# Performance work log

Hardware: AMD Instinct MI355X
Metric: run time of the kernel (lower is better)

## Reference

```python
import jax, jax.numpy as jnp
import numpy as np

B, S, HID = 1, 2048, 4096
NH, NKV, HD = 32, 8, 128
GROUPS = NH // NKV
EPS = 1e-8
THETA = 10000.0
SCALE = HD ** -0.5
INIT = 0.02


def setup_inputs() -> dict:
    key = jax.random.key(0)
    ks = jax.random.split(key, 8)
    return {
        "hidden_states": jax.random.normal(ks[0], (B, S, HID), jnp.float32),
        "position_ids": jnp.arange(S, dtype=jnp.int32)[None, :],
        "wq": jax.random.normal(ks[1], (HID, NH * HD), jnp.float32) * INIT,
        "wk": jax.random.normal(ks[2], (HID, NKV * HD), jnp.float32) * INIT,
        "wv": jax.random.normal(ks[3], (HID, NKV * HD), jnp.float32) * INIT,
        "wo": jax.random.normal(ks[4], (NH * HD, HID), jnp.float32) * INIT,
        "memory": jax.random.normal(ks[5], (NKV, HD, HD), jnp.float32) * INIT,
        "norm_m": jax.random.uniform(ks[6], (NKV, HD, HD), jnp.float32) * 0.5 + 0.5,
        "beta": jnp.zeros((1,), jnp.float32),
    }


def _rotate_half(x):
    h = x.shape[-1] // 2
    return jnp.concatenate([-x[..., h:], x[..., :h]], axis=-1)


def _rope(position_ids):
    inv_freq = 1.0 / (THETA ** (jnp.arange(0, HD, 2, dtype=jnp.float32) / HD))  # [HD/2]
    freqs = position_ids.astype(jnp.float32)[:, :, None] * inv_freq[None, None, :]  # [B,S,HD/2]
    emb = jnp.concatenate([freqs, freqs], axis=-1)  # [B,S,HD]
    return jnp.cos(emb)[:, None], jnp.sin(emb)[:, None]  # [B,1,S,HD] each


def reference(hidden_states, position_ids, wq, wk, wv, wo, memory, norm_m, beta):
    # projections -> [B, heads, S, HD]
    q = (hidden_states @ wq).reshape(B, S, NH, HD).transpose(0, 2, 1, 3)
    k = (hidden_states @ wk).reshape(B, S, NKV, HD).transpose(0, 2, 1, 3)
    v = (hidden_states @ wv).reshape(B, S, NKV, HD).transpose(0, 2, 1, 3)

    # ---- retrieve from compressive memory (pre-RoPE Q, as in original) ----
    qf = jax.nn.elu(q) + 1.0
    qn = qf / (qf.sum(axis=-1, keepdims=True) + EPS)            # [B,NH,S,HD]
    mem_t = jnp.tile(memory[None], (1, GROUPS, 1, 1))            # torch .repeat == tile: head h -> memory[h % NKV]
    norm_t = jnp.tile(jnp.swapaxes(norm_m, -1, -2)[None], (1, GROUPS, 1, 1))
    mem_out = jnp.matmul(qn, mem_t) / (jnp.matmul(qn, norm_t) + EPS)  # [B,NH,S,HD]

    # ---- delta-rule memory update (no-grad side effect in torch) ----
    kf = jax.nn.elu(k) + 1.0
    kn = kf / (kf.sum(axis=-1, keepdims=True) + EPS)             # [B,NKV,S,HD]
    v_ret = jnp.matmul(kn, memory) / (jnp.matmul(kn, jnp.swapaxes(norm_m, -1, -2)) + EPS)
    delta = jnp.einsum('bhsd,bhse->hde', kn, v - v_ret)          # sum over batch
    updated_memory = memory + delta
    updated_norm = norm_m + kn.sum(axis=2, keepdims=True)[0]     # [NKV,1,HD] broadcast

    # ---- RoPE ----
    cos, sin = _rope(position_ids)
    q = q * cos + _rotate_half(q) * sin
    k = k * cos + _rotate_half(k) * sin

    # ---- causal attention with GQA (repeat_interleave for K/V) ----
    kr = jnp.repeat(k, GROUPS, axis=1)
    vr = jnp.repeat(v, GROUPS, axis=1)
    scores = jnp.einsum('bhqd,bhkd->bhqk', q, kr) * SCALE        # [B,NH,S,S]
    causal = jnp.tril(jnp.ones((S, S), dtype=bool))
    scores = jnp.where(causal, scores, jnp.finfo(scores.dtype).min)
    attn = jax.nn.softmax(scores, axis=-1)
    attn_out = jnp.einsum('bhqk,bhkd->bhqd', attn, vr)           # [B,NH,S,HD]

    # ---- sigmoid-gated combine + output projection ----
    gate = jax.nn.sigmoid(beta)                                   # [1]
    combined = gate * mem_out + (1.0 - gate) * attn_out
    out = combined.transpose(0, 2, 1, 3).reshape(B, S, NH * HD) @ wo
    return out, updated_memory, updated_norm
```

## Files before the change

kernel.cpp:

```cpp
#include <hip/hip_runtime.h>

#define S_LEN 2048
#define HID_DIM 4096
#define NH 32
#define NKV 8
#define HD 128
#define QKV_N 6144
#define SCALE_F 0.08838834764831845f

typedef unsigned short u16;
typedef __attribute__((ext_vector_type(8))) __bf16 bf16x8;
typedef __attribute__((ext_vector_type(4))) float f32x4;

__device__ __forceinline__ u16 f2bf(float f) {
  unsigned u = __float_as_uint(f);
  return (u16)((u + 0x7fffu + ((u >> 16) & 1u)) >> 16);
}
__device__ __forceinline__ float bf2f(u16 v) {
  return __uint_as_float((unsigned)v << 16);
}

__device__ __forceinline__ void gl_lds16(const u16* g, u16* l) {
  __builtin_amdgcn_global_load_lds(
      (const __attribute__((address_space(1))) unsigned int*)g,
      (__attribute__((address_space(3))) unsigned int*)l, 16, 0, 0);
}


__device__ __forceinline__ void tr64_body(const float* __restrict__ A, u16* __restrict__ O,
                                          int ld_in, int ld_out, int r0, int c0, int tid) {
  __shared__ float tile[64][65];
  int tx = tid & 31, ty = tid >> 5;
#pragma unroll
  for (int i = 0; i < 8; i++) {
    int r = ty + 8 * i;
    float2 v = *(const float2*)&A[(long)(r0 + r) * ld_in + c0 + 2 * tx];
    tile[r][2 * tx] = v.x;
    tile[r][2 * tx + 1] = v.y;
  }
  __syncthreads();
#pragma unroll
  for (int i = 0; i < 8; i++) {
    int c = ty + 8 * i;
    ushort2 o;
    o.x = f2bf(tile[2 * tx][c]);
    o.y = f2bf(tile[2 * tx + 1][c]);
    *(ushort2*)&O[(long)(c0 + c) * ld_out + r0 + 2 * tx] = o;
  }
}

__device__ __forceinline__ void tr64u_body(const u16* __restrict__ A, u16* __restrict__ O,
                                           int ld_in, int ld_out, int r0, int c0, int tid) {
  __shared__ u16 tileu[64][66];
  int tx = tid & 31, ty = tid >> 5;
#pragma unroll
  for (int i = 0; i < 8; i++) {
    int r = ty + 8 * i;
    ushort2 v = *(const ushort2*)&A[(long)(r0 + r) * ld_in + c0 + 2 * tx];
    tileu[r][2 * tx] = v.x;
    tileu[r][2 * tx + 1] = v.y;
  }
  __syncthreads();
#pragma unroll
  for (int i = 0; i < 8; i++) {
    int c = ty + 8 * i;
    ushort2 o;
    o.x = tileu[2 * tx][c];
    o.y = tileu[2 * tx + 1][c];
    *(ushort2*)&O[(long)(c0 + c) * ld_out + r0 + 2 * tx] = o;
  }
}

__global__ void k_tr64(const float* __restrict__ in, u16* __restrict__ out,
                       int ld_in, int ld_out, long in_bs, long out_bs) {
  tr64_body(in + (long)blockIdx.z * in_bs, out + (long)blockIdx.z * out_bs,
            ld_in, ld_out, blockIdx.y * 64, blockIdx.x * 64, threadIdx.x);
}

__global__ void k_prep(const float* __restrict__ hs, u16* __restrict__ hsb,
                       const float* __restrict__ wq, const float* __restrict__ wk,
                       const float* __restrict__ wv, u16* __restrict__ wT6) {
  int bid = blockIdx.x;
  if (bid < 6144) {
    const float* src; int ld, bx, by; long ooff;
    if (bid < 4096) { src = wq; ld = 4096; ooff = 0; bx = bid & 63; by = bid >> 6; }
    else if (bid < 5120) { int b = bid - 4096; src = wk; ld = 1024; ooff = (long)4096 * HID_DIM; bx = b & 15; by = b >> 4; }
    else { int b = bid - 5120; src = wv; ld = 1024; ooff = (long)5120 * HID_DIM; bx = b & 15; by = b >> 4; }
    tr64_body(src, wT6 + ooff, ld, HID_DIM, by * 64, bx * 64, threadIdx.x);
  } else {
    long i = (long)(bid - 6144) * 256 + threadIdx.x;
    float4 v = ((const float4*)hs)[i];
    ushort4 o;
    o.x = f2bf(v.x); o.y = f2bf(v.y); o.z = f2bf(v.z); o.w = f2bf(v.w);
    ((ushort4*)hsb)[i] = o;
  }
}

__global__ void k_mid(const u16* __restrict__ qkvb, u16* __restrict__ vtb,
                      const float* __restrict__ memf, const float* __restrict__ norm,
                      u16* __restrict__ bc) {
  int bid = blockIdx.x;
  if (bid < 512) {
    int z = bid >> 6, sub = bid & 63;
    int bx = sub & 1, by = sub >> 1;
    tr64u_body(qkvb + HID_DIM + NKV * HD + z * HD, vtb + (long)z * HD * S_LEN,
               QKV_N, S_LEN, by * 64, bx * 64, threadIdx.x);
  } else if (bid < 544) {
    int b = bid - 512;
    int h = b >> 2, sub = b & 3;
    tr64_body(memf + (long)h * HD * HD, bc + (long)h * 32768,
              HD, HD, (sub >> 1) * 64, (sub & 1) * 64, threadIdx.x);
  } else {
    int cid = bid - 544;
    int h = cid >> 6, chunk = cid & 63;
    int i = chunk * 256 + threadIdx.x;
    bc[(long)h * 32768 + 16384 + i] = f2bf(norm[(long)h * 16384 + i]);
  }
}


template <int BN>
__global__ __launch_bounds__(512, 2) void k_gemm8(
    const u16* __restrict__ A, const u16* __restrict__ A2, int zsplit,
    const u16* __restrict__ Bt, void* __restrict__ Cv,
    int kloop, int lda, int ldb, int ldc,
    long strideA, long strideB, long strideC, int bmodB, int obf) {
  constexpr int NBG = BN / 64;
  constexpr int NNI = BN / 64;
  constexpr int BSTRIDE = 16384 + BN * 64;
  __shared__ __align__(16) u16 lds[2 * BSTRIDE];
  const int bz = blockIdx.z;
  const u16* Ap = (bz < zsplit) ? (A + (long)bz * strideA)
                                : (A2 + (long)(bz - zsplit) * strideA);
  const u16* Bp = Bt + (long)(bz % bmodB) * strideB;
  const long coff = (long)bz * strideC;

  const int gx = gridDim.x, gy = gridDim.y;
  const int nwg = gx * gy;
  int id = blockIdx.y * gx + blockIdx.x;
  if (!(nwg & 7)) { int q = nwg >> 3; id = (id & 7) * q + (id >> 3); }
  const int m0 = (id % gy) * 256;
  const int n0 = (id / gy) * BN;

  const int tid = threadIdx.x, wid = tid >> 6, lane = tid & 63;
  const int l15 = lane & 15, lhi = lane >> 4;
  const int wm = wid >> 2, wn = wid & 3;

  const int srow = (wid << 3) + (lane >> 3);
  const int ssw = ((lane & 7) ^ (lane >> 3)) * 8;
  auto stA = [&](int d, int g, long kt) {
    gl_lds16(Ap + (long)(m0 + g * 64 + srow) * lda + kt + ssw,
             &lds[d * BSTRIDE + (g * 64 + (wid << 3)) * 64]);
  };
  auto stB = [&](int d, int g, long kt) {
    gl_lds16(Bp + (long)(n0 + g * 64 + srow) * ldb + kt + ssw,
             &lds[d * BSTRIDE + 16384 + (g * 64 + (wid << 3)) * 64]);
  };

  const int swb = l15 & 7;
  const int aBase = (wm * 128 + l15) * 64;
  const int bBase = 16384 + (wn * (BN / 4) + l15) * 64;
  const int ko0 = (lhi ^ swb) * 8;
  const int ko1 = ((4 + lhi) ^ swb) * 8;

  const int KT = kloop >> 6;
  const int NIT = KT >> 1;

  f32x4 acc[8][NNI];
#pragma unroll
  for (int i = 0; i < 8; i++)
#pragma unroll
    for (int j = 0; j < NNI; j++) acc[i][j] = (f32x4){0.f, 0.f, 0.f, 0.f};

#pragma unroll
  for (int g = 0; g < 4; g++) stA(0, g, 0);
#pragma unroll
  for (int g = 0; g < NBG; g++) stB(0, g, 0);
#pragma unroll
  for (int g = 0; g < NBG; g++) stB(1, g, 64);
  asm volatile("s_waitcnt vmcnt(%0)" :: "i"(NBG) : "memory");
  __builtin_amdgcn_s_barrier();
  asm volatile("" ::: "memory");

  for (int t = 0; t < NIT; ++t) {
    const long kA = (long)(2 * t + 1) * 64;
    const long kB0 = (long)(2 * t + 2) * 64;
    const long kB1 = (long)(2 * t + 3) * 64;
    const bool st0 = (2 * t + 2) < KT;
    const bool st1 = (2 * t + 3) < KT;
    const bool last = (t + 1 == NIT);

    {
      const u16* lb = &lds[0];
      bf16x8 Bf[NNI][2];
#pragma unroll
      for (int p = 0; p < 4; p++) {
        if (p == 0) {
#pragma unroll
          for (int ni = 0; ni < NNI; ni++) {
            Bf[ni][0] = *(const bf16x8*)&lb[bBase + ni * 1024 + ko0];
            Bf[ni][1] = *(const bf16x8*)&lb[bBase + ni * 1024 + ko1];
          }
        }
        bf16x8 a0k0 = *(const bf16x8*)&lb[aBase + (2 * p) * 1024 + ko0];
        bf16x8 a0k1 = *(const bf16x8*)&lb[aBase + (2 * p) * 1024 + ko1];
        bf16x8 a1k0 = *(const bf16x8*)&lb[aBase + (2 * p + 1) * 1024 + ko0];
        bf16x8 a1k1 = *(const bf16x8*)&lb[aBase + (2 * p + 1) * 1024 + ko1];
        if (p == 0) { stA(1, 0, kA); stA(1, 1, kA); }
        else if (p == 1) { stA(1, 2, kA); stA(1, 3, kA); }
        else if (p == 2) { if (st0) { stB(0, 0, kB0); stB(0, 1, kB0); } }
        else {
          if (st0) { stB(0, 2, kB0); if (NBG > 3) stB(0, 3, kB0); }
        }
        asm volatile("" ::: "memory");
        if (p == 3) {
          if (last) asm volatile("s_waitcnt vmcnt(0)" ::: "memory");
          else      asm volatile("s_waitcnt vmcnt(%0)" :: "i"(NBG) : "memory");
        }
        __builtin_amdgcn_s_barrier();
        asm volatile("" ::: "memory");
        __builtin_amdgcn_s_setprio(1);
#pragma unroll
        for (int ni = 0; ni < NNI; ni++) {
          acc[2 * p][ni] = __builtin_amdgcn_mfma_f32_16x16x32_bf16(a0k0, Bf[ni][0], acc[2 * p][ni], 0, 0, 0);
          acc[2 * p][ni] = __builtin_amdgcn_mfma_f32_16x16x32_bf16(a0k1, Bf[ni][1], acc[2 * p][ni], 0, 0, 0);
          acc[2 * p + 1][ni] = __builtin_amdgcn_mfma_f32_16x16x32_bf16(a1k0, Bf[ni][0], acc[2 * p + 1][ni], 0, 0, 0);
          acc[2 * p + 1][ni] = __builtin_amdgcn_mfma_f32_16x16x32_bf16(a1k1, Bf[ni][1], acc[2 * p + 1][ni], 0, 0, 0);
        }
        __builtin_amdgcn_s_setprio(0);
        asm volatile("" ::: "memory");
        __builtin_amdgcn_s_barrier();
        asm volatile("" ::: "memory");
      }
    }
    {
      const u16* lb = &lds[BSTRIDE];
      bf16x8 Bf[NNI][2];
#pragma unroll
      for (int p = 0; p < 4; p++) {
        if (p == 0) {
#pragma unroll
          for (int ni = 0; ni < NNI; ni++) {
            Bf[ni][0] = *(const bf16x8*)&lb[bBase + ni * 1024 + ko0];
            Bf[ni][1] = *(const bf16x8*)&lb[bBase + ni * 1024 + ko1];
          }
        }
        bf16x8 a0k0 = *(const bf16x8*)&lb[aBase + (2 * p) * 1024 + ko0];
        bf16x8 a0k1 = *(const bf16x8*)&lb[aBase + (2 * p) * 1024 + ko1];
        bf16x8 a1k0 = *(const bf16x8*)&lb[aBase + (2 * p + 1) * 1024 + ko0];
        bf16x8 a1k1 = *(const bf16x8*)&lb[aBase + (2 * p + 1) * 1024 + ko1];
        if (p == 0) { if (st0) { stA(0, 0, kB0); stA(0, 1, kB0); } }
        else if (p == 1) { if (st0) { stA(0, 2, kB0); stA(0, 3, kB0); } }
        else if (p == 2) { if (st1) { stB(1, 0, kB1); stB(1, 1, kB1); } }
        else {
          if (st1) { stB(1, 2, kB1); if (NBG > 3) stB(1, 3, kB1); }
        }
        asm volatile("" ::: "memory");
        if (p == 3 && !last)
          asm volatile("s_waitcnt vmcnt(%0)" :: "i"(NBG) : "memory");
        __builtin_amdgcn_s_barrier();
        asm volatile("" ::: "memory");
        __builtin_amdgcn_s_setprio(1);
#pragma unroll
        for (int ni = 0; ni < NNI; ni++) {
          acc[2 * p][ni] = __builtin_amdgcn_mfma_f32_16x16x32_bf16(a0k0, Bf[ni][0], acc[2 * p][ni], 0, 0, 0);
          acc[2 * p][ni] = __builtin_amdgcn_mfma_f32_16x16x32_bf16(a0k1, Bf[ni][1], acc[2 * p][ni], 0, 0, 0);
          acc[2 * p + 1][ni] = __builtin_amdgcn_mfma_f32_16x16x32_bf16(a1k0, Bf[ni][0], acc[2 * p + 1][ni], 0, 0, 0);
          acc[2 * p + 1][ni] = __builtin_amdgcn_mfma_f32_16x16x32_bf16(a1k1, Bf[ni][1], acc[2 * p + 1][ni], 0, 0, 0);
        }
        __builtin_amdgcn_s_setprio(0);
        asm volatile("" ::: "memory");
        __builtin_amdgcn_s_barrier();
        asm volatile("" ::: "memory");
      }
    }
  }

#pragma unroll
  for (int mi = 0; mi < 8; mi++)
#pragma unroll
    for (int ni = 0; ni < NNI; ni++)
#pragma unroll
      for (int j = 0; j < 4; j++) {
        long row = m0 + wm * 128 + mi * 16 + lhi * 4 + j;
        long col = n0 + wn * (BN / 4) + ni * 16 + l15;
        if (obf)
          ((u16*)Cv)[coff + row * ldc + col] = f2bf(acc[mi][ni][j]);
        else
          ((float*)Cv)[coff + row * ldc + col] = acc[mi][ni][j];
      }
}


__global__ void k_addp(const u16* __restrict__ p0, const u16* __restrict__ p1,
                       float* __restrict__ out) {
  long i = ((long)blockIdx.x * 256 + threadIdx.x) * 8;
  ushort4 a0 = *(const ushort4*)&p0[i], a1 = *(const ushort4*)&p0[i + 4];
  ushort4 b0 = *(const ushort4*)&p1[i], b1 = *(const ushort4*)&p1[i + 4];
  float4 o0, o1;
  o0.x = bf2f(a0.x) + bf2f(b0.x); o0.y = bf2f(a0.y) + bf2f(b0.y);
  o0.z = bf2f(a0.z) + bf2f(b0.z); o0.w = bf2f(a0.w) + bf2f(b0.w);
  o1.x = bf2f(a1.x) + bf2f(b1.x); o1.y = bf2f(a1.y) + bf2f(b1.y);
  o1.z = bf2f(a1.z) + bf2f(b1.z); o1.w = bf2f(a1.w) + bf2f(b1.w);
  *(float4*)&out[i] = o0;
  *(float4*)&out[i + 4] = o1;
}


__global__ void k_qnrope(const u16* __restrict__ qkv, const int* __restrict__ pos,
                         u16* __restrict__ qnb, u16* __restrict__ qrb,
                         u16* __restrict__ knb, u16* __restrict__ krb) {
  int s = blockIdx.x, y = blockIdx.y, l = threadIdx.x;
  bool isq = y < NH;
  int h = isq ? y : y - NH;
  const u16* row = qkv + (long)s * QKV_N + (isq ? h * HD : HID_DIM + h * HD);
  float x0 = bf2f(row[l]), x1 = bf2f(row[l + 64]);
  float f0 = x0 > 0.f ? x0 + 1.f : __expf(x0);
  float f1 = x1 > 0.f ? x1 + 1.f : __expf(x1);
  float sum = f0 + f1;
#pragma unroll
  for (int m = 32; m >= 1; m >>= 1) sum += __shfl_xor(sum, m);
  float inv = 1.f / (sum + 1e-8f);
  float y0 = f0 * inv, y1 = f1 * inv;
  long o = ((long)h * S_LEN + s) * HD;
  float p = (float)pos[s];
  float ang = p * expf(-(float)l * (9.210340371976184f / 64.0f));
  float c = cosf(ang), sn = sinf(ang);
  u16 r0 = f2bf(x0 * c - x1 * sn), r1 = f2bf(x1 * c + x0 * sn);
  if (isq) {
    qnb[o + l] = f2bf(y0); qnb[o + l + 64] = f2bf(y1);
    qrb[o + l] = r0; qrb[o + l + 64] = r1;
  } else {
    knb[o + l] = f2bf(y0); knb[o + l + 64] = f2bf(y1);
    krb[o + l] = r0; krb[o + l + 64] = r1;
  }
}


__global__ __launch_bounds__(256, 2) void k_flash4(
    const u16* __restrict__ qr, const u16* __restrict__ kr,
    const u16* __restrict__ vt, const u16* __restrict__ rawq,
    const float* __restrict__ beta, u16* __restrict__ comb) {
  __shared__ u16 KV[2][16384];
  __shared__ u16 Ps[4][16 * 64];
  const int bx = blockIdx.x, h = blockIdx.y;
  const int hk = h >> 2;
  const int tid = threadIdx.x, wid = tid >> 6, lane = tid & 63;
  const int l15 = lane & 15, lhi = lane >> 4;
  const u16* qbase = qr + (long)h * S_LEN * HD;
  const u16* kb0 = kr + (long)hk * S_LEN * HD;
  const u16* vb0 = vt + (long)hk * HD * S_LEN;
  u16* P = Ps[wid];
  const float g = 1.f / (1.f + __expf(-beta[0]));

  int kr_r[4], kr_sc[4], vr_r[4], vr_sc[4];
#pragma unroll
  for (int it = 0; it < 4; it++) {
    int chunk = it * 4 + wid;
    kr_r[it] = chunk * 4 + (lane >> 4);
    kr_sc[it] = ((lane & 15) * 8) ^ ((kr_r[it] & 7) * 8);
    vr_r[it] = chunk * 8 + (lane >> 3);
    vr_sc[it] = ((lane & 7) * 8) ^ ((vr_r[it] & 7) * 8);
  }

  for (int si = 0; si < 2; si++) {
    const int s = si ? (31 - bx) : bx;
    const int qs = s * 64 + wid * 16;
    bf16x8 aq[4];
#pragma unroll
    for (int kc = 0; kc < 4; kc++)
      aq[kc] = *(const bf16x8*)&qbase[(long)(qs + l15) * HD + kc * 32 + lhi * 8];
    f32x4 accO[8];
#pragma unroll
    for (int i = 0; i < 8; i++) accO[i] = (f32x4){0.f, 0.f, 0.f, 0.f};
    float rs[4] = {0.f, 0.f, 0.f, 0.f};

    if (si) __syncthreads();
    {
      u16* Kb = KV[0];
#pragma unroll
      for (int it = 0; it < 4; it++)
        gl_lds16(kb0 + (long)kr_r[it] * HD + kr_sc[it], &Kb[(it * 4 + wid) * 512]);
#pragma unroll
      for (int it = 0; it < 4; it++)
        gl_lds16(vb0 + (long)vr_r[it] * S_LEN + vr_sc[it], &Kb[8192 + (it * 4 + wid) * 512]);
    }
    int cur = 0;

    for (int t = 0; t <= s; t++) {
      asm volatile("s_waitcnt vmcnt(0)" ::: "memory");
      __syncthreads();
      if (t < s) {
        u16* Kb = KV[cur ^ 1];
        const long kt = (long)(t + 1) * 64;
#pragma unroll
        for (int it = 0; it < 4; it++)
          gl_lds16(kb0 + (kt + kr_r[it]) * HD + kr_sc[it], &Kb[(it * 4 + wid) * 512]);
#pragma unroll
        for (int it = 0; it < 4; it++)
          gl_lds16(vb0 + (long)vr_r[it] * S_LEN + kt + vr_sc[it], &Kb[8192 + (it * 4 + wid) * 512]);
      }
      const u16* Ks = KV[cur];
      const u16* Vs = Ks + 8192;

      f32x4 accS[4];
#pragma unroll
      for (int i = 0; i < 4; i++) accS[i] = (f32x4){0.f, 0.f, 0.f, 0.f};
#pragma unroll
      for (int ni = 0; ni < 4; ni++) {
        int row = ni * 16 + l15;
#pragma unroll
        for (int kc = 0; kc < 4; kc++) {
          bf16x8 bk = *(const bf16x8*)&Ks[row * 128 + ((kc * 32 + lhi * 8) ^ ((row & 7) * 8))];
          accS[ni] = __builtin_amdgcn_mfma_f32_16x16x32_bf16(aq[kc], bk, accS[ni], 0, 0, 0);
        }
      }
      const bool diag = (t == s);
#pragma unroll
      for (int ni = 0; ni < 4; ni++) {
        int col = t * 64 + ni * 16 + l15;
#pragma unroll
        for (int j = 0; j < 4; j++) {
          int row = qs + lhi * 4 + j;
          float p = (!diag || col <= row) ? __expf(accS[ni][j] * SCALE_F) : 0.f;
          rs[j] += p;
          int pr = lhi * 4 + j;
          P[pr * 64 + ((ni * 16 + l15) ^ ((pr & 7) * 8))] = f2bf(p);
        }
      }
      asm volatile("s_waitcnt lgkmcnt(0)" ::: "memory");
      __builtin_amdgcn_sched_barrier(0);
      bf16x8 ap[2];
#pragma unroll
      for (int ks = 0; ks < 2; ks++)
        ap[ks] = *(const bf16x8*)&P[l15 * 64 + ((ks * 32 + lhi * 8) ^ ((l15 & 7) * 8))];
#pragma unroll
      for (int nj = 0; nj < 8; nj++) {
        int row = nj * 16 + l15;
#pragma unroll
        for (int ks = 0; ks < 2; ks++) {
          bf16x8 bv = *(const bf16x8*)&Vs[row * 64 + ((ks * 32 + lhi * 8) ^ ((row & 7) * 8))];
          accO[nj] = __builtin_amdgcn_mfma_f32_16x16x32_bf16(ap[ks], bv, accO[nj], 0, 0, 0);
        }
      }
      cur ^= 1;
    }
#pragma unroll
    for (int j = 0; j < 4; j++) {
      float v = rs[j];
      v += __shfl_xor(v, 1);
      v += __shfl_xor(v, 2);
      v += __shfl_xor(v, 4);
      v += __shfl_xor(v, 8);
      rs[j] = 1.f / v;
    }
#pragma unroll
    for (int nj = 0; nj < 8; nj++)
#pragma unroll
      for (int j = 0; j < 4; j++) {
        int row = qs + lhi * 4 + j;
        int col = nj * 16 + l15;
        long rb = ((long)h * S_LEN + row) * 256 + col;
        float mo = bf2f(rawq[rb]) / (bf2f(rawq[rb + 128]) + 1e-8f);
        float ao = accO[nj][j] * rs[j];
        comb[(long)row * HID_DIM + h * HD + col] = f2bf(g * mo + (1.f - g) * ao);
      }
  }
}


__global__ __launch_bounds__(256) void k_delta_part(
    const u16* __restrict__ knb, const u16* __restrict__ rawk,
    const u16* __restrict__ qkvb,
    float* __restrict__ dpart, float* __restrict__ npart) {
  __shared__ float knc[64][128];
  __shared__ u16 Uc[64][128];
  const int h = blockIdx.x, c = blockIdx.y, t = threadIdx.x;
  const long rb = ((long)h * S_LEN + (long)c * 64) * HD;
  const long rkb = ((long)h * S_LEN + (long)c * 64) * 256;
  const u16* vb = qkvb + HID_DIM + NKV * HD + h * HD + (long)c * 64 * QKV_N;
  for (int i = t; i < 1024; i += 256) {
    int r = i >> 4, cb = (i & 15) * 8;
    ushort4 k0 = *(const ushort4*)&knb[rb + (long)r * HD + cb];
    ushort4 k1 = *(const ushort4*)&knb[rb + (long)r * HD + cb + 4];
    knc[r][cb + 0] = bf2f(k0.x); knc[r][cb + 1] = bf2f(k0.y);
    knc[r][cb + 2] = bf2f(k0.z); knc[r][cb + 3] = bf2f(k0.w);
    knc[r][cb + 4] = bf2f(k1.x); knc[r][cb + 5] = bf2f(k1.y);
    knc[r][cb + 6] = bf2f(k1.z); knc[r][cb + 7] = bf2f(k1.w);
    ushort4 n0 = *(const ushort4*)&rawk[rkb + (long)r * 256 + cb];
    ushort4 n1 = *(const ushort4*)&rawk[rkb + (long)r * 256 + cb + 4];
    ushort4 dn0 = *(const ushort4*)&rawk[rkb + (long)r * 256 + 128 + cb];
    ushort4 dn1 = *(const ushort4*)&rawk[rkb + (long)r * 256 + 128 + cb + 4];
    ushort4 v0 = *(const ushort4*)&vb[(long)r * QKV_N + cb];
    ushort4 v1 = *(const ushort4*)&vb[(long)r * QKV_N + cb + 4];
    ushort4 u0, u1;
    u0.x = f2bf(bf2f(v0.x) - bf2f(n0.x) / (bf2f(dn0.x) + 1e-8f));
    u0.y = f2bf(bf2f(v0.y) - bf2f(n0.y) / (bf2f(dn0.y) + 1e-8f));
    u0.z = f2bf(bf2f(v0.z) - bf2f(n0.z) / (bf2f(dn0.z) + 1e-8f));
    u0.w = f2bf(bf2f(v0.w) - bf2f(n0.w) / (bf2f(dn0.w) + 1e-8f));
    u1.x = f2bf(bf2f(v1.x) - bf2f(n1.x) / (bf2f(dn1.x) + 1e-8f));
    u1.y = f2bf(bf2f(v1.y) - bf2f(n1.y) / (bf2f(dn1.y) + 1e-8f));
    u1.z = f2bf(bf2f(v1.z) - bf2f(n1.z) / (bf2f(dn1.z) + 1e-8f));
    u1.w = f2bf(bf2f(v1.w) - bf2f(n1.w) / (bf2f(dn1.w) + 1e-8f));
    *(ushort4*)&Uc[r][cb] = u0;
    *(ushort4*)&Uc[r][cb + 4] = u1;
  }
  __syncthreads();

  const int e = t & 127, dh = (t >> 7) * 64;
  float acc[64];
#pragma unroll
  for (int d = 0; d < 64; d++) acc[d] = 0.f;
  for (int s = 0; s < 64; s++) {
    float u = bf2f(Uc[s][e]);
#pragma unroll
    for (int dq = 0; dq < 16; dq++) {
      float4 k4 = *(const float4*)&knc[s][dh + dq * 4];
      acc[dq * 4 + 0] += k4.x * u;
      acc[dq * 4 + 1] += k4.y * u;
      acc[dq * 4 + 2] += k4.z * u;
      acc[dq * 4 + 3] += k4.w * u;
    }
  }
  long ob = (((long)c * NKV + h) * 128 + dh) * 128 + e;
#pragma unroll
  for (int d = 0; d < 64; d++) dpart[ob + (long)d * 128] = acc[d];

  {
    int j = e, half = t >> 7;
    float cs = 0.f;
#pragma unroll
    for (int s = 0; s < 32; s++) cs += knc[half * 32 + s][j];
    npart[(((long)c * 2 + half) * NKV + h) * 128 + j] = cs;
  }
}

__global__ void k_finish(const float* __restrict__ dpart, const float* __restrict__ npart,
                         const float* __restrict__ mem, const float* __restrict__ norm,
                         float* __restrict__ outmem, float* __restrict__ outn) {
  int bid = blockIdx.x;
  if (bid < 512) {
    long i = (long)bid * 256 + threadIdx.x;
    const long N = (long)NKV * HD * HD;
    float a = 0.f;
#pragma unroll 8
    for (int c = 0; c < 32; c++) a += dpart[(long)c * N + i];
    outmem[i] = mem[i] + a;
  } else {
    int b2 = bid - 512;
    int h = b2 >> 6, y = b2 & 63;
    int j = threadIdx.x & 127;
    int r = y * 2 + (threadIdx.x >> 7);
    float cs = 0.f;
#pragma unroll 8
    for (int cc = 0; cc < 64; cc++) cs += npart[((long)cc * NKV + h) * 128 + j];
    long o = (long)h * HD * HD + (long)r * HD + j;
    outn[o] = norm[o] + cs;
  }
}


extern "C" void kernel_launch(void* const* d_in, const int* in_sizes, int n_in,
                              void* d_out, int out_size, void* d_ws, size_t ws_size,
                              hipStream_t stream) {
  const float* hs = (const float*)d_in[0];
  const int* pos = (const int*)d_in[1];
  const float* wq = (const float*)d_in[2];
  const float* wk = (const float*)d_in[3];
  const float* wv = (const float*)d_in[4];
  const float* wo = (const float*)d_in[5];
  const float* memf = (const float*)d_in[6];
  const float* normf = (const float*)d_in[7];
  const float* beta = (const float*)d_in[8];
  (void)in_sizes; (void)n_in; (void)out_size; (void)ws_size;

  float* out = (float*)d_out;
  float* out_mem = out + (long)S_LEN * HID_DIM;
  float* out_norm = out_mem + NKV * HD * HD;

  const size_t MB = 1u << 20;
  char* w = (char*)d_ws;
  u16* hsb    = (u16*)(w + 0);
  u16* qnb    = (u16*)(w + 0);
  u16* comb   = (u16*)(w + 0);
  u16* wT6    = (u16*)(w + 16 * MB);
  u16* rawq   = (u16*)(w + 16 * MB);
  u16* woT    = (u16*)(w + 16 * MB);
  u16* rawk   = (u16*)(w + 48 * MB);
  u16* bc     = (u16*)(w + 57 * MB);
  u16* vtb    = (u16*)(w + 57 * MB + 512 * 1024);
  u16* qkvb   = (u16*)(w + 66 * MB + 512 * 1024);
  u16* p0     = (u16*)(w + 90 * MB + 512 * 1024);
  u16* qrb    = (u16*)(w + 130 * MB + 512 * 1024);
  float* dpart= (float*)(w + 130 * MB + 512 * 1024);
  u16* p1     = (u16*)(w + 130 * MB + 512 * 1024);
  u16* krb    = (u16*)(w + 146 * MB + 512 * 1024);
  float* npart= (float*)(w + 146 * MB + 512 * 1024);
  u16* knb    = (u16*)(w + 150 * MB + 512 * 1024);

  k_prep<<<dim3(14336), dim3(256), 0, stream>>>(hs, hsb, wq, wk, wv, wT6);
  k_gemm8<192><<<dim3(QKV_N / 192, S_LEN / 256, 1), dim3(512), 0, stream>>>(
      hsb, hsb, 1 << 30, wT6, qkvb, HID_DIM, HID_DIM, HID_DIM, QKV_N,
      0L, 0L, 0L, 1, 1);

  k_qnrope<<<dim3(S_LEN, NH + NKV), dim3(64), 0, stream>>>(
      qkvb, pos, qnb, qrb, knb, krb);

  k_mid<<<dim3(1056), dim3(256), 0, stream>>>(qkvb, vtb, memf, normf, bc);

  k_gemm8<256><<<dim3(1, 8, NH + NKV), dim3(512), 0, stream>>>(
      qnb, knb, NH, bc, rawq, HD, HD, HD, 256,
      (long)(S_LEN * HD), (long)(256 * HD), (long)(S_LEN * 256), NKV, 1);

  k_flash4<<<dim3(16, NH), dim3(256), 0, stream>>>(qrb, krb, vtb, rawq, beta, comb);

  k_delta_part<<<dim3(NKV, 32), dim3(256), 0, stream>>>(knb, rawk, qkvb, dpart, npart);
  k_finish<<<dim3(1024), dim3(256), 0, stream>>>(dpart, npart, memf, normf, out_mem, out_norm);

  k_tr64<<<dim3(64, 64, 1), dim3(256), 0, stream>>>(
      wo, woT, HID_DIM, HID_DIM, 0L, 0L);
  k_gemm8<256><<<dim3(HID_DIM / 256, S_LEN / 256, 2), dim3(512), 0, stream>>>(
      comb, comb, 1 << 30, woT, p0, 2048, HID_DIM, HID_DIM, HID_DIM,
      2048L, 2048L, (long)(p1 - p0), 2, 1);
  k_addp<<<dim3(S_LEN * HID_DIM / 2048), dim3(256), 0, stream>>>(p0, p1, out);
}
```

Baseline: 356.5 us.

## Triple-buffer the A operand in the QKV projection GEMM to prefetch further ahead

Adds a template parameter to the GEMM kernel so the A tile can use a ring of ATRI LDS buffers, separate from the double-buffered B tiles. The QKV projection instantiates it with three A buffers, so A loads are issued two k-steps ahead, with vmcnt wait counts adjusted to match. The aim is to hide global load latency for A. The cost is more LDS per block (3*32KB for A plus 2*24KB for B), which may cut occupancy below the two blocks per CU requested by the launch bounds.

```diff
diff --git a/kernel.cpp b/kernel.cpp
--- a/kernel.cpp
+++ b/kernel.cpp
@@ -119,7 +119,7 @@
 }
 
 
-template <int BN>
+template <int BN, int ATRI>
 __global__ __launch_bounds__(512, 2) void k_gemm8(
     const u16* __restrict__ A, const u16* __restrict__ A2, int zsplit,
     const u16* __restrict__ Bt, void* __restrict__ Cv,
@@ -127,8 +127,12 @@
     long strideA, long strideB, long strideC, int bmodB, int obf) {
   constexpr int NBG = BN / 64;
   constexpr int NNI = BN / 64;
-  constexpr int BSTRIDE = 16384 + BN * 64;
-  __shared__ __align__(16) u16 lds[2 * BSTRIDE];
+  constexpr int AHEAD = ATRI - 1;
+  constexpr int WAITN = NBG + 4 * (AHEAD - 1);
+  constexpr int AELT = 16384;
+  constexpr int ABYTES = ATRI * AELT;
+  constexpr int BN64 = BN * 64;
+  __shared__ __align__(16) u16 lds[ABYTES + 2 * BN64];
   const int bz = blockIdx.z;
   const u16* Ap = (bz < zsplit) ? (A + (long)bz * strideA)
                                 : (A2 + (long)(bz - zsplit) * strideA);
@@ -148,18 +152,18 @@
 
   const int srow = (wid << 3) + (lane >> 3);
   const int ssw = ((lane & 7) ^ (lane >> 3)) * 8;
-  auto stA = [&](int d, int g, long kt) {
+  auto stA = [&](int ab, int g, long kt) {
     gl_lds16(Ap + (long)(m0 + g * 64 + srow) * lda + kt + ssw,
-             &lds[d * BSTRIDE + (g * 64 + (wid << 3)) * 64]);
+             &lds[ab * AELT + (g * 64 + (wid << 3)) * 64]);
   };
   auto stB = [&](int d, int g, long kt) {
     gl_lds16(Bp + (long)(n0 + g * 64 + srow) * ldb + kt + ssw,
-             &lds[d * BSTRIDE + 16384 + (g * 64 + (wid << 3)) * 64]);
+             &lds[ABYTES + d * BN64 + (g * 64 + (wid << 3)) * 64]);
   };
 
   const int swb = l15 & 7;
   const int aBase = (wm * 128 + l15) * 64;
-  const int bBase = 16384 + (wn * (BN / 4) + l15) * 64;
+  const int bBase = (wn * (BN / 4) + l15) * 64;
   const int ko0 = (lhi ^ swb) * 8;
   const int ko1 = ((4 + lhi) ^ swb) * 8;
 
@@ -176,46 +180,58 @@
   for (int g = 0; g < 4; g++) stA(0, g, 0);
 #pragma unroll
   for (int g = 0; g < NBG; g++) stB(0, g, 0);
+  if (ATRI > 2) {
+#pragma unroll
+    for (int g = 0; g < 4; g++) stA(1, g, 64);
+  }
 #pragma unroll
   for (int g = 0; g < NBG; g++) stB(1, g, 64);
-  asm volatile("s_waitcnt vmcnt(%0)" :: "i"(NBG) : "memory");
+  asm volatile("s_waitcnt vmcnt(%0)" :: "i"(WAITN) : "memory");
   __builtin_amdgcn_s_barrier();
   asm volatile("" ::: "memory");
 
+  int ab0 = 0;
   for (int t = 0; t < NIT; ++t) {
-    const long kA = (long)(2 * t + 1) * 64;
+    const int uS0 = 2 * t + AHEAD;
+    const int uS1 = 2 * t + 1 + AHEAD;
+    const int abR0 = ab0;
+    const int abR1 = (ab0 + 1 < ATRI) ? (ab0 + 1) : 0;
+    const int abS0 = (ab0 + AHEAD < ATRI) ? (ab0 + AHEAD) : (ab0 + AHEAD - ATRI);
+    const int abS1 = (abS0 + 1 < ATRI) ? (abS0 + 1) : 0;
+    const long kA0 = (long)uS0 * 64, kA1 = (long)uS1 * 64;
     const long kB0 = (long)(2 * t + 2) * 64;
     const long kB1 = (long)(2 * t + 3) * 64;
-    const bool st0 = (2 * t + 2) < KT;
-    const bool st1 = (2 * t + 3) < KT;
+    const bool sA0 = uS0 < KT, sA1 = uS1 < KT;
+    const bool sB0 = (2 * t + 2) < KT, sB1 = (2 * t + 3) < KT;
     const bool last = (t + 1 == NIT);
 
     {
-      const u16* lb = &lds[0];
+      const u16* la = &lds[abR0 * AELT];
+      const u16* lbB = &lds[ABYTES];
       bf16x8 Bf[NNI][2];
 #pragma unroll
       for (int p = 0; p < 4; p++) {
         if (p == 0) {
 #pragma unroll
           for (int ni = 0; ni < NNI; ni++) {
-            Bf[ni][0] = *(const bf16x8*)&lb[bBase + ni * 1024 + ko0];
-            Bf[ni][1] = *(const bf16x8*)&lb[bBase + ni * 1024 + ko1];
+            Bf[ni][0] = *(const bf16x8*)&lbB[bBase + ni * 1024 + ko0];
+            Bf[ni][1] = *(const bf16x8*)&lbB[bBase + ni * 1024 + ko1];
           }
         }
-        bf16x8 a0k0 = *(const bf16x8*)&lb[aBase + (2 * p) * 1024 + ko0];
-        bf16x8 a0k1 = *(const bf16x8*)&lb[aBase + (2 * p) * 1024 + ko1];
-        bf16x8 a1k0 = *(const bf16x8*)&lb[aBase + (2 * p + 1) * 1024 + ko0];
-        bf16x8 a1k1 = *(const bf16x8*)&lb[aBase + (2 * p + 1) * 1024 + ko1];
-        if (p == 0) { stA(1, 0, kA); stA(1, 1, kA); }
-        else if (p == 1) { stA(1, 2, kA); stA(1, 3, kA); }
-        else if (p == 2) { if (st0) { stB(0, 0, kB0); stB(0, 1, kB0); } }
+        bf16x8 a0k0 = *(const bf16x8*)&la[aBase + (2 * p) * 1024 + ko0];
+        bf16x8 a0k1 = *(const bf16x8*)&la[aBase + (2 * p) * 1024 + ko1];
+        bf16x8 a1k0 = *(const bf16x8*)&la[aBase + (2 * p + 1) * 1024 + ko0];
+        bf16x8 a1k1 = *(const bf16x8*)&la[aBase + (2 * p + 1) * 1024 + ko1];
+        if (p == 0) { if (sA0) { stA(abS0, 0, kA0); stA(abS0, 1, kA0); } }
+        else if (p == 1) { if (sA0) { stA(abS0, 2, kA0); stA(abS0, 3, kA0); } }
+        else if (p == 2) { if (sB0) { stB(0, 0, kB0); stB(0, 1, kB0); } }
         else {
-          if (st0) { stB(0, 2, kB0); if (NBG > 3) stB(0, 3, kB0); }
+          if (sB0) { stB(0, 2, kB0); if (NBG > 3) stB(0, 3, kB0); }
         }
         asm volatile("" ::: "memory");
         if (p == 3) {
           if (last) asm volatile("s_waitcnt vmcnt(0)" ::: "memory");
-          else      asm volatile("s_waitcnt vmcnt(%0)" :: "i"(NBG) : "memory");
+          else      asm volatile("s_waitcnt vmcnt(%0)" :: "i"(WAITN) : "memory");
         }
         __builtin_amdgcn_s_barrier();
         asm volatile("" ::: "memory");
@@ -234,30 +250,31 @@
       }
     }
     {
-      const u16* lb = &lds[BSTRIDE];
+      const u16* la = &lds[abR1 * AELT];
+      const u16* lbB = &lds[ABYTES + BN64];
       bf16x8 Bf[NNI][2];
 #pragma unroll
       for (int p = 0; p < 4; p++) {
         if (p == 0) {
 #pragma unroll
           for (int ni = 0; ni < NNI; ni++) {
-            Bf[ni][0] = *(const bf16x8*)&lb[bBase + ni * 1024 + ko0];
-            Bf[ni][1] = *(const bf16x8*)&lb[bBase + ni * 1024 + ko1];
+            Bf[ni][0] = *(const bf16x8*)&lbB[bBase + ni * 1024 + ko0];
+            Bf[ni][1] = *(const bf16x8*)&lbB[bBase + ni * 1024 + ko1];
           }
         }
-        bf16x8 a0k0 = *(const bf16x8*)&lb[aBase + (2 * p) * 1024 + ko0];
-        bf16x8 a0k1 = *(const bf16x8*)&lb[aBase + (2 * p) * 1024 + ko1];
-        bf16x8 a1k0 = *(const bf16x8*)&lb[aBase + (2 * p + 1) * 1024 + ko0];
-        bf16x8 a1k1 = *(const bf16x8*)&lb[aBase + (2 * p + 1) * 1024 + ko1];
-        if (p == 0) { if (st0) { stA(0, 0, kB0); stA(0, 1, kB0); } }
-        else if (p == 1) { if (st0) { stA(0, 2, kB0); stA(0, 3, kB0); } }
-        else if (p == 2) { if (st1) { stB(1, 0, kB1); stB(1, 1, kB1); } }
+        bf16x8 a0k0 = *(const bf16x8*)&la[aBase + (2 * p) * 1024 + ko0];
+        bf16x8 a0k1 = *(const bf16x8*)&la[aBase + (2 * p) * 1024 + ko1];
+        bf16x8 a1k0 = *(const bf16x8*)&la[aBase + (2 * p + 1) * 1024 + ko0];
+        bf16x8 a1k1 = *(const bf16x8*)&la[aBase + (2 * p + 1) * 1024 + ko1];
+        if (p == 0) { if (sA1) { stA(abS1, 0, kA1); stA(abS1, 1, kA1); } }
+        else if (p == 1) { if (sA1) { stA(abS1, 2, kA1); stA(abS1, 3, kA1); } }
+        else if (p == 2) { if (sB1) { stB(1, 0, kB1); stB(1, 1, kB1); } }
         else {
-          if (st1) { stB(1, 2, kB1); if (NBG > 3) stB(1, 3, kB1); }
+          if (sB1) { stB(1, 2, kB1); if (NBG > 3) stB(1, 3, kB1); }
         }
         asm volatile("" ::: "memory");
         if (p == 3 && !last)
-          asm volatile("s_waitcnt vmcnt(%0)" :: "i"(NBG) : "memory");
+          asm volatile("s_waitcnt vmcnt(%0)" :: "i"(WAITN) : "memory");
         __builtin_amdgcn_s_barrier();
         asm volatile("" ::: "memory");
         __builtin_amdgcn_s_setprio(1);
@@ -274,6 +291,7 @@
         asm volatile("" ::: "memory");
       }
     }
+    ab0 = (ab0 + 2 < ATRI) ? (ab0 + 2) : (ab0 + 2 - ATRI);
   }
 
 #pragma unroll
@@ -599,7 +617,7 @@
   u16* knb    = (u16*)(w + 150 * MB + 512 * 1024);
 
   k_prep<<<dim3(14336), dim3(256), 0, stream>>>(hs, hsb, wq, wk, wv, wT6);
-  k_gemm8<192><<<dim3(QKV_N / 192, S_LEN / 256, 1), dim3(512), 0, stream>>>(
+  k_gemm8<192, 3><<<dim3(QKV_N / 192, S_LEN / 256, 1), dim3(512), 0, stream>>>(
       hsb, hsb, 1 << 30, wT6, qkvb, HID_DIM, HID_DIM, HID_DIM, QKV_N,
       0L, 0L, 0L, 1, 1);
 
@@ -608,7 +626,7 @@
 
   k_mid<<<dim3(1056), dim3(256), 0, stream>>>(qkvb, vtb, memf, normf, bc);
 
-  k_gemm8<256><<<dim3(1, 8, NH + NKV), dim3(512), 0, stream>>>(
+  k_gemm8<256, 2><<<dim3(1, 8, NH + NKV), dim3(512), 0, stream>>>(
       qnb, knb, NH, bc, rawq, HD, HD, HD, 256,
       (long)(S_LEN * HD), (long)(256 * HD), (long)(S_LEN * 256), NKV, 1);
 
@@ -619,7 +637,7 @@
 
   k_tr64<<<dim3(64, 64, 1), dim3(256), 0, stream>>>(
       wo, woT, HID_DIM, HID_DIM, 0L, 0L);
-  k_gemm8<256><<<dim3(HID_DIM / 256, S_LEN / 256, 2), dim3(512), 0, stream>>>(
+  k_gemm8<256, 2><<<dim3(HID_DIM / 256, S_LEN / 256, 2), dim3(512), 0, stream>>>(
       comb, comb, 1 << 30, woT, p0, 2048, HID_DIM, HID_DIM, HID_DIM,
       2048L, 2048L, (long)(p1 - p0), 2, 1);
   k_addp<<<dim3(S_LEN * HID_DIM / 2048), dim3(256), 0, stream>>>(p0, p1, out);
```

Measured after the change: 357.4 us. About the same (+0.2%).
